# Kernel tuning notes

Hardware: AMD Instinct MI355X
Metric: run time of the kernel (lower is better)

The kernel has to match this reference:

```python
import jax, jax.numpy as jnp
import numpy as np
import math

BIG, SMALL, HEADS, FF_MULT = 4096, 256, 4, 2
HEAD_DIM = SMALL // HEADS
FF = SMALL * FF_MULT
EPS = 1.1920929e-07  # torch.nn.RMSNorm default eps=None -> finfo(float32).eps


def rmsnorm(x, g):
    var = jnp.mean(x * x, axis=-1, keepdims=True)
    return x * jax.lax.rsqrt(var + EPS) * g


def setup_inputs() -> dict:
    key = jax.random.key(0)
    ks = jax.random.split(key, 10)
    B, T = 4, 2048
    def lin(k, out_d, in_d):
        # torch nn.Linear default init: U(-1/sqrt(in), 1/sqrt(in)), weight shape (out, in)
        lim = 1.0 / math.sqrt(in_d)
        return jax.random.uniform(k, (out_d, in_d), jnp.float32, -lim, lim)
    return {
        "x": jax.random.normal(ks[0], (B, T, BIG), jnp.float32),
        "W_down": lin(ks[1], SMALL, BIG),
        "W_up": lin(ks[2], BIG, SMALL),
        "W_qkv": lin(ks[3], 3 * SMALL, SMALL),
        "W_o": lin(ks[4], SMALL, SMALL),
        "W_gate": lin(ks[5], FF, SMALL),
        "W_upff": lin(ks[6], FF, SMALL),
        "W_downff": lin(ks[7], SMALL, FF),
        "g1": jnp.ones((SMALL,), jnp.float32),
        "g2": jnp.ones((SMALL,), jnp.float32),
    }


def reference(x, W_down, W_up, W_qkv, W_o, W_gate, W_upff, W_downff, g1, g2):
    B, T, _ = x.shape
    h = x @ W_down.T                                     # (B,T,small)
    hn = rmsnorm(h, g1)
    qkv = (hn @ W_qkv.T).reshape(B, T, 3, HEADS, HEAD_DIM)
    qkv = jnp.transpose(qkv, (2, 0, 3, 1, 4))            # (3,B,H,T,hd)
    q, k, v = qkv[0], qkv[1], qkv[2]
    scores = jnp.einsum('bhqd,bhkd->bhqk', q, k) / math.sqrt(HEAD_DIM)
    causal = jnp.tril(jnp.ones((T, T), bool))
    scores = jnp.where(causal, scores, -jnp.inf)
    attn = jax.nn.softmax(scores, axis=-1)
    out = jnp.einsum('bhqk,bhkd->bhqd', attn, v)
    out = jnp.transpose(out, (0, 2, 1, 3)).reshape(B, T, SMALL)
    h = h + out @ W_o.T
    hn = rmsnorm(h, g2)
    ff = (jax.nn.silu(hn @ W_gate.T) * (hn @ W_upff.T)) @ W_downff.T
    h = h + ff
    return h @ W_up.T                                    # (B,T,big)
```

## Files before the change

kernel.cpp:

```cpp
#include <hip/hip_runtime.h>
#include <hip/hip_bf16.h>

typedef __bf16 bf16x8 __attribute__((ext_vector_type(8)));
typedef __bf16 bf16x4 __attribute__((ext_vector_type(4)));
typedef float f32x4 __attribute__((ext_vector_type(4)));

#define MFMA_BF16(a, b, c) __builtin_amdgcn_mfma_f32_16x16x32_bf16((a), (b), (c), 0, 0, 0)

__device__ __forceinline__ void g2lds16(void* lds, const void* g) {
  __builtin_amdgcn_global_load_lds(
      (const __attribute__((address_space(1))) void*)g,
      (__attribute__((address_space(3))) void*)lds, 16, 0, 0);
}

enum { EP_BF16 = 0, EP_F32 = 1, EP_ADD_F32 = 2, EP_ADD_BF16OUT = 3 };

template <int EPI, int MT, bool SPLITK = false>
__global__ __launch_bounds__(256, 2) void gemm_nt_kernel(
    const __bf16* __restrict__ A, const __bf16* __restrict__ B, const int K,
    __bf16* __restrict__ Co, float* __restrict__ Cf, const int ldc)
{
  __shared__ __align__(16) __bf16 As[2][MT * 32];
  __shared__ __align__(16) __bf16 Bs[2][128 * 32];
  const int tid = threadIdx.x;
  const int wv = tid >> 6, lane = tid & 63;
  const int r16 = lane & 15, g4 = lane >> 4;
  const int row0 = blockIdx.y * MT, col0 = blockIdx.x * 128;
  const int wr = (MT == 128) ? (wv >> 1) * 64 : 0;
  const int wc = (MT == 128) ? (wv & 1) * 64 : wv * 32;
  constexpr int NW = (MT == 128) ? 4 : 2;
  constexpr int NA = (MT == 128) ? 2 : 1;
  const int kz0 = SPLITK ? blockIdx.z * 512 : 0;

  f32x4 acc[4][NW];
#pragma unroll
  for (int m = 0; m < 4; ++m)
#pragma unroll
    for (int n = 0; n < NW; ++n) acc[m][n] = f32x4{0.f, 0.f, 0.f, 0.f};

  auto stage = [&](int buf, int k0) {
#pragma unroll
    for (int rr = 0; rr < NA; ++rr) {
      const int u = rr * 256 + tid, row = u >> 2, cg = ((u & 3) ^ (row & 3)) * 8;
      g2lds16(&As[buf][u * 8], A + (size_t)(row0 + row) * K + k0 + cg);
    }
#pragma unroll
    for (int rr = 0; rr < 2; ++rr) {
      const int u = rr * 256 + tid, row = u >> 2, cg = ((u & 3) ^ (row & 3)) * 8;
      g2lds16(&Bs[buf][u * 8], B + (size_t)(col0 + row) * K + k0 + cg);
    }
  };

  const int nk = SPLITK ? 16 : (K >> 5);
  const int csw = (g4 ^ (r16 & 3)) * 8;
  int cur = 0;
  stage(0, kz0);
  __syncthreads();

  for (int t = 0; t < nk; ++t) {
    if (t + 1 < nk) stage(cur ^ 1, kz0 + (t + 1) * 32);
    bf16x8 af[4], bfr[NW];
#pragma unroll
    for (int m = 0; m < 4; ++m)
      af[m] = *(const bf16x8*)&As[cur][(wr + m * 16 + r16) * 32 + csw];
#pragma unroll
    for (int n = 0; n < NW; ++n)
      bfr[n] = *(const bf16x8*)&Bs[cur][(wc + n * 16 + r16) * 32 + csw];
#pragma unroll
    for (int m = 0; m < 4; ++m)
#pragma unroll
      for (int n = 0; n < NW; ++n)
        acc[m][n] = MFMA_BF16(af[m], bfr[n], acc[m][n]);
    __syncthreads();
    cur ^= 1;
  }

  const size_t zoff = SPLITK ? (size_t)blockIdx.z * 2097152 : 0;
#pragma unroll
  for (int m = 0; m < 4; ++m)
#pragma unroll
    for (int n = 0; n < NW; ++n)
#pragma unroll
      for (int r = 0; r < 4; ++r) {
        const int row = row0 + wr + m * 16 + g4 * 4 + r;
        const int col = col0 + wc + n * 16 + r16;
        const size_t idx = (size_t)row * ldc + col;
        const float v = acc[m][n][r];
        if constexpr (EPI == EP_BF16) Co[zoff + idx] = (__bf16)v;
        else if constexpr (EPI == EP_F32) Cf[idx] = v;
        else if constexpr (EPI == EP_ADD_F32) Cf[idx] += v;
        else Co[idx] = (__bf16)(Cf[idx] + v);
      }
}

__global__ void cvt_x_kernel(const float* __restrict__ src, __bf16* __restrict__ dst)
{
  const int stride = gridDim.x * 256;
  for (size_t i = (size_t)blockIdx.x * 256 + threadIdx.x; i < 8388608; i += stride) {
    const f32x4 v = *(const f32x4*)(src + i * 4);
    bf16x4 o;
#pragma unroll
    for (int j = 0; j < 4; ++j) o[j] = (__bf16)v[j];
    *(bf16x4*)(dst + i * 4) = o;
  }
}

__global__ void rmsnorm_reduce_kernel(const __bf16* __restrict__ part, const float* __restrict__ g,
                                      float* __restrict__ h, __bf16* __restrict__ out)
{
  const int wv = threadIdx.x >> 6, lane = threadIdx.x & 63;
  const size_t row = (size_t)blockIdx.x * 4 + wv;
  const size_t i = row * 256 + lane * 4;
  f32x4 v = {0.f, 0.f, 0.f, 0.f};
#pragma unroll
  for (int z = 0; z < 8; ++z) {
    const bf16x4 p = *(const bf16x4*)(part + (size_t)z * 2097152 + i);
#pragma unroll
    for (int j = 0; j < 4; ++j) v[j] += (float)p[j];
  }
  *(f32x4*)(h + i) = v;
  float s = v[0] * v[0] + v[1] * v[1] + v[2] * v[2] + v[3] * v[3];
#pragma unroll
  for (int off = 1; off < 64; off <<= 1) s += __shfl_xor(s, off);
  const float scale = rsqrtf(s * (1.f / 256.f) + 1.1920929e-07f);
  const f32x4 gv = *(const f32x4*)(g + lane * 4);
  bf16x4 o;
#pragma unroll
  for (int j = 0; j < 4; ++j) o[j] = (__bf16)(v[j] * scale * gv[j]);
  *(bf16x4*)(out + i) = o;
}

__global__ void rmsnorm_kernel(const float* __restrict__ h, const float* __restrict__ g,
                               __bf16* __restrict__ out)
{
  const int wv = threadIdx.x >> 6, lane = threadIdx.x & 63;
  const size_t row = (size_t)blockIdx.x * 4 + wv;
  const f32x4 v = *(const f32x4*)(h + row * 256 + lane * 4);
  float s = v[0] * v[0] + v[1] * v[1] + v[2] * v[2] + v[3] * v[3];
#pragma unroll
  for (int off = 1; off < 64; off <<= 1) s += __shfl_xor(s, off);
  const float scale = rsqrtf(s * (1.f / 256.f) + 1.1920929e-07f);
  const f32x4 gv = *(const f32x4*)(g + lane * 4);
  bf16x4 o;
#pragma unroll
  for (int j = 0; j < 4; ++j) o[j] = (__bf16)(v[j] * scale * gv[j]);
  *(bf16x4*)(out + row * 256 + lane * 4) = o;
}

struct CvtPack { const float* s[7]; __bf16* d[7]; int n[7]; };
__global__ void cvt_all_kernel(CvtPack p)
{
  int i = (blockIdx.x * 256 + threadIdx.x) * 4;
#pragma unroll
  for (int k = 0; k < 7; ++k) {
    if (i < p.n[k]) {
      const f32x4 v = *(const f32x4*)(p.s[k] + i);
      bf16x4 o;
#pragma unroll
      for (int j = 0; j < 4; ++j) o[j] = (__bf16)v[j];
      *(bf16x4*)(p.d[k] + i) = o;
      return;
    }
    i -= p.n[k];
  }
}

__global__ void silumul_kernel(const __bf16* __restrict__ gu, __bf16* __restrict__ out)
{
  const int gid = blockIdx.x * 256 + threadIdx.x;
  const int row = gid >> 6, k = (gid & 63) * 8;
  const bf16x8 gv = *(const bf16x8*)(gu + (size_t)row * 1024 + k);
  const bf16x8 uv = *(const bf16x8*)(gu + (size_t)row * 1024 + 512 + k);
  bf16x8 ov;
#pragma unroll
  for (int j = 0; j < 8; ++j) {
    const float x = (float)gv[j];
    ov[j] = (__bf16)((x / (1.f + __expf(-x))) * (float)uv[j]);
  }
  *(bf16x8*)(out + (size_t)row * 512 + k) = ov;
}

__global__ __launch_bounds__(256, 4) void attn_kernel(
    const __bf16* __restrict__ qkv, float* __restrict__ opart, float* __restrict__ lpart)
{
  const int bh = blockIdx.x;
  const int by = blockIdx.y;
  const int qb = (by < 16) ? (31 - by) : (by - 16);
  const int z = blockIdx.z;
  const int b = bh >> 2, hh = bh & 3;
  const int tid = threadIdx.x, wv = tid >> 6, lane = tid & 63;
  const int r16 = lane & 15, g4 = lane >> 4;
  const __bf16* base = qkv + (size_t)b * 2048 * 768;
  const int q0 = qb * 64;

  __shared__ __align__(16) __bf16 Ks[2][64 * 64];
  __shared__ __align__(16) __bf16 Vt[64 * 72];
  __shared__ __align__(16) __bf16 Ps[4][16 * 72];

  bf16x8 qf[2];
  {
    const __bf16* qrow = base + (size_t)(q0 + wv * 16 + r16) * 768 + hh * 64;
    qf[0] = *(const bf16x8*)(qrow + g4 * 8);
    qf[1] = *(const bf16x8*)(qrow + 32 + g4 * 8);
  }

  f32x4 oacc[4];
#pragma unroll
  for (int t = 0; t < 4; ++t) oacc[t] = f32x4{0.f, 0.f, 0.f, 0.f};
  float lsum[4] = {0.f, 0.f, 0.f, 0.f};

  auto stageK = [&](int buf, int kv0) {
#pragma unroll
    for (int rr = 0; rr < 2; ++rr) {
      const int u = rr * 256 + tid;
      const int kv = u >> 3, c = u & 7;
      g2lds16(&Ks[buf][u * 8],
              base + (size_t)(kv0 + kv) * 768 + 256 + hh * 64 + ((c ^ (kv & 7)) * 8));
    }
  };
  const int vrow = tid >> 2, vdg = (tid & 3) * 16;
  const int va_ = vrow >> 3, vb_ = vrow & 7;

  bf16x8 v0r, v1r;
  auto loadV = [&](int kv0) {
    const __bf16* vsrc = base + (size_t)(kv0 + vrow) * 768 + 512 + hh * 64 + vdg;
    v0r = *(const bf16x8*)vsrc;
    v1r = *(const bf16x8*)(vsrc + 8);
  };
  auto writeVt = [&]() {
#pragma unroll
    for (int i = 0; i < 8; ++i) {
      int d = vdg + i;
      Vt[d * 72 + ((va_ ^ (d >> 3)) << 3) + vb_] = v0r[i];
      d = vdg + 8 + i;
      Vt[d * 72 + ((va_ ^ (d >> 3)) << 3) + vb_] = v1r[i];
    }
  };

  int c = z, cur = 0;
  const bool any = (c <= qb);
  if (any) { stageK(0, c * 64); loadV(c * 64); }
  __syncthreads();
  if (any) writeVt();
  __syncthreads();

  while (c <= qb) {
    const int nxt = c + 2;
    if (nxt <= qb) { stageK(cur ^ 1, nxt * 64); loadV(nxt * 64); }

    f32x4 sacc[4];
#pragma unroll
    for (int t = 0; t < 4; ++t) sacc[t] = f32x4{0.f, 0.f, 0.f, 0.f};
#pragma unroll
    for (int t = 0; t < 4; ++t)
#pragma unroll
      for (int kk = 0; kk < 2; ++kk) {
        const bf16x8 kf = *(const bf16x8*)
            &Ks[cur][(t * 16 + r16) * 64 + (((kk * 4 + g4) ^ (r16 & 7)) * 8)];
        sacc[t] = MFMA_BF16(qf[kk], kf, sacc[t]);
      }

    const bool diag = (c == qb);
#pragma unroll
    for (int t = 0; t < 4; ++t)
#pragma unroll
      for (int r = 0; r < 4; ++r) {
        float p = __expf(sacc[t][r] * 0.125f);
        if (diag && (t * 16 + r16 > wv * 16 + g4 * 4 + r)) p = 0.f;
        lsum[r] += p;
        Ps[wv][(g4 * 4 + r) * 72 + t * 16 + r16] = (__bf16)p;
      }
    bf16x8 pa[2];
    pa[0] = *(const bf16x8*)&Ps[wv][r16 * 72 + g4 * 8];
    pa[1] = *(const bf16x8*)&Ps[wv][r16 * 72 + 32 + g4 * 8];

#pragma unroll
    for (int t2 = 0; t2 < 4; ++t2)
#pragma unroll
      for (int kk = 0; kk < 2; ++kk) {
        const int d = t2 * 16 + r16;
        const bf16x8 vf = *(const bf16x8*)
            &Vt[d * 72 + (((kk * 4 + g4) ^ (d >> 3)) * 8)];
        oacc[t2] = MFMA_BF16(pa[kk], vf, oacc[t2]);
      }

    __syncthreads();
    if (nxt <= qb) writeVt();
    __syncthreads();
    c = nxt;
    cur ^= 1;
  }

#pragma unroll
  for (int r = 0; r < 4; ++r) {
    lsum[r] += __shfl_xor(lsum[r], 1);
    lsum[r] += __shfl_xor(lsum[r], 2);
    lsum[r] += __shfl_xor(lsum[r], 4);
    lsum[r] += __shfl_xor(lsum[r], 8);
  }
  const size_t pb = (size_t)(bh * 32 + qb) * 2 + z;
  float* op = opart + pb * 4096;
#pragma unroll
  for (int t2 = 0; t2 < 4; ++t2)
#pragma unroll
    for (int r = 0; r < 4; ++r)
      op[(wv * 16 + g4 * 4 + r) * 64 + t2 * 16 + r16] = oacc[t2][r];
  if (r16 == 0) {
    float* lp = lpart + pb * 64;
#pragma unroll
    for (int r = 0; r < 4; ++r) lp[wv * 16 + g4 * 4 + r] = lsum[r];
  }
}

__global__ void attn_merge_kernel(const float* __restrict__ opart,
                                  const float* __restrict__ lpart,
                                  __bf16* __restrict__ ao)
{
  const int gid = blockIdx.x * 256 + threadIdx.x;
  const int col4 = (gid & 63) * 4;
  const int row_t = gid >> 6;
  const int b = row_t >> 11, row = row_t & 2047;
  const int qb = row >> 6, rloc = row & 63;
  const int hh = col4 >> 6, d = col4 & 63;
  const size_t p0 = ((size_t)((b * 4 + hh) * 32 + qb)) * 2;
  const f32x4 o0 = *(const f32x4*)(opart + p0 * 4096 + rloc * 64 + d);
  const f32x4 o1 = *(const f32x4*)(opart + (p0 + 1) * 4096 + rloc * 64 + d);
  const float inv = 1.f / (lpart[p0 * 64 + rloc] + lpart[(p0 + 1) * 64 + rloc]);
  bf16x4 o;
#pragma unroll
  for (int j = 0; j < 4; ++j) o[j] = (__bf16)((o0[j] + o1[j]) * inv);
  *(bf16x4*)(ao + (size_t)row_t * 256 + col4) = o;
}

extern "C" void kernel_launch(void* const* d_in, const int* in_sizes, int n_in,
                              void* d_out, int out_size, void* d_ws, size_t ws_size,
                              hipStream_t stream) {
  (void)in_sizes; (void)n_in; (void)out_size; (void)ws_size;
  const float* x     = (const float*)d_in[0];
  const float* Wdown = (const float*)d_in[1];
  const float* Wup   = (const float*)d_in[2];
  const float* Wqkv  = (const float*)d_in[3];
  const float* Wo    = (const float*)d_in[4];
  const float* Wgate = (const float*)d_in[5];
  const float* Wupff = (const float*)d_in[6];
  const float* Wdff  = (const float*)d_in[7];
  const float* g1    = (const float*)d_in[8];
  const float* g2    = (const float*)d_in[9];
  float* out = (float*)d_out;

  const size_t MB = 1 << 20;
  char* ws = (char*)d_ws;
  float*  h  = (float*)ws;
  __bf16* hn = (__bf16*)(ws + 8 * MB);
  __bf16* ao = (__bf16*)(ws + 12 * MB);
  __bf16* wb_down = (__bf16*)(ws + 16 * MB);
  __bf16* wb_up   = (__bf16*)(ws + 18 * MB);
  __bf16* wb_qkv  = (__bf16*)(ws + 20 * MB);
  __bf16* wb_o    = (__bf16*)(ws + 20 * MB + 384 * 1024);
  __bf16* wb_gate = (__bf16*)(ws + 20 * MB + 512 * 1024);
  __bf16* wb_upff = (__bf16*)(ws + 20 * MB + 768 * 1024);
  __bf16* wb_dff  = (__bf16*)(ws + 21 * MB);
  __bf16* hb = ao;

  char* ob = (char*)d_out;
  __bf16* xb    = (__bf16*)(ob);
  __bf16* hpart = (__bf16*)(ob + 64 * MB);
  __bf16* qkv   = (__bf16*)(ob);
  __bf16* gu    = (__bf16*)(ob + 12 * MB);
  __bf16* ffmid = (__bf16*)(ob + 28 * MB);
  float* opart  = (float*)(ob + 36 * MB);
  float* lpart  = (float*)(ob + 53 * MB);

  CvtPack cp;
  cp.s[0] = Wdown; cp.d[0] = wb_down; cp.n[0] = 1048576;
  cp.s[1] = Wup;   cp.d[1] = wb_up;   cp.n[1] = 1048576;
  cp.s[2] = Wqkv;  cp.d[2] = wb_qkv;  cp.n[2] = 196608;
  cp.s[3] = Wo;    cp.d[3] = wb_o;    cp.n[3] = 65536;
  cp.s[4] = Wgate; cp.d[4] = wb_gate; cp.n[4] = 131072;
  cp.s[5] = Wupff; cp.d[5] = wb_upff; cp.n[5] = 131072;
  cp.s[6] = Wdff;  cp.d[6] = wb_dff;  cp.n[6] = 131072;
  cvt_all_kernel<<<2688, 256, 0, stream>>>(cp);

  cvt_x_kernel<<<2048, 256, 0, stream>>>(x, xb);
  gemm_nt_kernel<EP_BF16, 128, true><<<dim3(2, 64, 8), 256, 0, stream>>>(
      xb, wb_down, 4096, hpart, nullptr, 256);
  rmsnorm_reduce_kernel<<<2048, 256, 0, stream>>>(hpart, g1, h, hn);

  gemm_nt_kernel<EP_BF16, 64><<<dim3(6, 128), 256, 0, stream>>>(
      hn, wb_qkv, 256, qkv, nullptr, 768);
  attn_kernel<<<dim3(16, 32, 2), 256, 0, stream>>>(qkv, opart, lpart);
  attn_merge_kernel<<<2048, 256, 0, stream>>>(opart, lpart, ao);
  gemm_nt_kernel<EP_ADD_F32, 64><<<dim3(2, 128), 256, 0, stream>>>(
      ao, wb_o, 256, nullptr, h, 256);
  rmsnorm_kernel<<<2048, 256, 0, stream>>>(h, g2, hn);
  gemm_nt_kernel<EP_BF16, 64><<<dim3(8, 128), 256, 0, stream>>>(
      hn, wb_gate, 256, gu, nullptr, 1024);
  silumul_kernel<<<2048, 256, 0, stream>>>(gu, ffmid);
  gemm_nt_kernel<EP_ADD_BF16OUT, 64><<<dim3(2, 128), 256, 0, stream>>>(
      ffmid, wb_dff, 512, hb, h, 256);
  gemm_nt_kernel<EP_F32, 128><<<dim3(32, 64), 256, 0, stream>>>(
      hb, wb_up, 256, nullptr, out, 4096);
}
```

Baseline: 213.1 us.

## Fuse attention merge into W_o GEMM, store bf16 partials, halve split-K

Removes the separate attention-merge kernel by merging the two split-KV partial outputs (now stored as bf16) and normalizing them during the A-tile load of a dedicated W_o GEMM. The down-projection split-K factor drops from 8 to 4, so the partial buffer and the reduce traffic shrink while each block runs a longer K loop. The final output GEMM uses nontemporal stores. This trades a kernel launch and fp32 partial traffic for non-async register-staged A loads and a small extra precision loss in the attention partials.

```diff
diff --git a/kernel.cpp b/kernel.cpp
--- a/kernel.cpp
+++ b/kernel.cpp
@@ -30,7 +30,7 @@
   const int wc = (MT == 128) ? (wv & 1) * 64 : wv * 32;
   constexpr int NW = (MT == 128) ? 4 : 2;
   constexpr int NA = (MT == 128) ? 2 : 1;
-  const int kz0 = SPLITK ? blockIdx.z * 512 : 0;
+  const int kz0 = SPLITK ? blockIdx.z * 1024 : 0;
 
   f32x4 acc[4][NW];
 #pragma unroll
@@ -51,7 +51,7 @@
     }
   };
 
-  const int nk = SPLITK ? 16 : (K >> 5);
+  const int nk = SPLITK ? 32 : (K >> 5);
   const int csw = (g4 ^ (r16 & 3)) * 8;
   int cur = 0;
   stage(0, kz0);
@@ -87,9 +87,89 @@
         const size_t idx = (size_t)row * ldc + col;
         const float v = acc[m][n][r];
         if constexpr (EPI == EP_BF16) Co[zoff + idx] = (__bf16)v;
-        else if constexpr (EPI == EP_F32) Cf[idx] = v;
+        else if constexpr (EPI == EP_F32) __builtin_nontemporal_store(v, &Cf[idx]);
         else if constexpr (EPI == EP_ADD_F32) Cf[idx] += v;
         else Co[idx] = (__bf16)(Cf[idx] + v);
+      }
+}
+
+__global__ __launch_bounds__(256, 2) void gemm_wo_kernel(
+    const __bf16* __restrict__ opart, const float* __restrict__ lpart,
+    const __bf16* __restrict__ B, float* __restrict__ Cf)
+{
+  __shared__ __align__(16) __bf16 As[2][64 * 32];
+  __shared__ __align__(16) __bf16 Bs[2][128 * 32];
+  const int tid = threadIdx.x;
+  const int wv = tid >> 6, lane = tid & 63;
+  const int r16 = lane & 15, g4 = lane >> 4;
+  const int row0 = blockIdx.y * 64, col0 = blockIdx.x * 128;
+  const int wc = wv * 32;
+
+  f32x4 acc[4][2];
+#pragma unroll
+  for (int m = 0; m < 4; ++m)
+#pragma unroll
+    for (int n = 0; n < 2; ++n) acc[m][n] = f32x4{0.f, 0.f, 0.f, 0.f};
+
+  const int arow = tid >> 2;
+  const int R = row0 + arow;
+  const int b = R >> 11, rr_ = R & 2047;
+  const int qb = rr_ >> 6, rloc = rr_ & 63;
+  const int cgrp = ((tid & 3) ^ (arow & 3)) * 8;
+
+  auto stageA = [&](int buf, int t) {
+    const int hh = t >> 1;
+    const int dbase = (t & 1) * 32 + cgrp;
+    const size_t pb = ((size_t)((b * 4 + hh) * 32 + qb)) * 2;
+    const bf16x8 o0 = *(const bf16x8*)(opart + pb * 4096 + rloc * 64 + dbase);
+    const bf16x8 o1 = *(const bf16x8*)(opart + (pb + 1) * 4096 + rloc * 64 + dbase);
+    const float inv = 1.f / (lpart[pb * 64 + rloc] + lpart[(pb + 1) * 64 + rloc]);
+    bf16x8 w;
+#pragma unroll
+    for (int j = 0; j < 8; ++j) w[j] = (__bf16)(((float)o0[j] + (float)o1[j]) * inv);
+    *(bf16x8*)&As[buf][tid * 8] = w;
+  };
+  auto stageB = [&](int buf, int k0) {
+#pragma unroll
+    for (int rr = 0; rr < 2; ++rr) {
+      const int u = rr * 256 + tid, row = u >> 2, cg = ((u & 3) ^ (row & 3)) * 8;
+      g2lds16(&Bs[buf][u * 8], B + (size_t)(col0 + row) * 256 + k0 + cg);
+    }
+  };
+
+  const int csw = (g4 ^ (r16 & 3)) * 8;
+  int cur = 0;
+  stageA(0, 0);
+  stageB(0, 0);
+  __syncthreads();
+
+  for (int t = 0; t < 8; ++t) {
+    if (t + 1 < 8) { stageA(cur ^ 1, t + 1); stageB(cur ^ 1, (t + 1) * 32); }
+    bf16x8 af[4], bfr[2];
+#pragma unroll
+    for (int m = 0; m < 4; ++m)
+      af[m] = *(const bf16x8*)&As[cur][(m * 16 + r16) * 32 + csw];
+#pragma unroll
+    for (int n = 0; n < 2; ++n)
+      bfr[n] = *(const bf16x8*)&Bs[cur][(wc + n * 16 + r16) * 32 + csw];
+#pragma unroll
+    for (int m = 0; m < 4; ++m)
+#pragma unroll
+      for (int n = 0; n < 2; ++n)
+        acc[m][n] = MFMA_BF16(af[m], bfr[n], acc[m][n]);
+    __syncthreads();
+    cur ^= 1;
+  }
+
+#pragma unroll
+  for (int m = 0; m < 4; ++m)
+#pragma unroll
+    for (int n = 0; n < 2; ++n)
+#pragma unroll
+      for (int r = 0; r < 4; ++r) {
+        const int row = row0 + m * 16 + g4 * 4 + r;
+        const int col = col0 + wc + n * 16 + r16;
+        Cf[(size_t)row * 256 + col] += acc[m][n][r];
       }
 }
 
@@ -113,7 +193,7 @@
   const size_t i = row * 256 + lane * 4;
   f32x4 v = {0.f, 0.f, 0.f, 0.f};
 #pragma unroll
-  for (int z = 0; z < 8; ++z) {
+  for (int z = 0; z < 4; ++z) {
     const bf16x4 p = *(const bf16x4*)(part + (size_t)z * 2097152 + i);
 #pragma unroll
     for (int j = 0; j < 4; ++j) v[j] += (float)p[j];
@@ -181,7 +261,7 @@
 }
 
 __global__ __launch_bounds__(256, 4) void attn_kernel(
-    const __bf16* __restrict__ qkv, float* __restrict__ opart, float* __restrict__ lpart)
+    const __bf16* __restrict__ qkv, __bf16* __restrict__ opart, float* __restrict__ lpart)
 {
   const int bh = blockIdx.x;
   const int by = blockIdx.y;
@@ -299,37 +379,17 @@
     lsum[r] += __shfl_xor(lsum[r], 8);
   }
   const size_t pb = (size_t)(bh * 32 + qb) * 2 + z;
-  float* op = opart + pb * 4096;
+  __bf16* op = opart + pb * 4096;
 #pragma unroll
   for (int t2 = 0; t2 < 4; ++t2)
 #pragma unroll
     for (int r = 0; r < 4; ++r)
-      op[(wv * 16 + g4 * 4 + r) * 64 + t2 * 16 + r16] = oacc[t2][r];
+      op[(wv * 16 + g4 * 4 + r) * 64 + t2 * 16 + r16] = (__bf16)oacc[t2][r];
   if (r16 == 0) {
     float* lp = lpart + pb * 64;
 #pragma unroll
     for (int r = 0; r < 4; ++r) lp[wv * 16 + g4 * 4 + r] = lsum[r];
   }
-}
-
-__global__ void attn_merge_kernel(const float* __restrict__ opart,
-                                  const float* __restrict__ lpart,
-                                  __bf16* __restrict__ ao)
-{
-  const int gid = blockIdx.x * 256 + threadIdx.x;
-  const int col4 = (gid & 63) * 4;
-  const int row_t = gid >> 6;
-  const int b = row_t >> 11, row = row_t & 2047;
-  const int qb = row >> 6, rloc = row & 63;
-  const int hh = col4 >> 6, d = col4 & 63;
-  const size_t p0 = ((size_t)((b * 4 + hh) * 32 + qb)) * 2;
-  const f32x4 o0 = *(const f32x4*)(opart + p0 * 4096 + rloc * 64 + d);
-  const f32x4 o1 = *(const f32x4*)(opart + (p0 + 1) * 4096 + rloc * 64 + d);
-  const float inv = 1.f / (lpart[p0 * 64 + rloc] + lpart[(p0 + 1) * 64 + rloc]);
-  bf16x4 o;
-#pragma unroll
-  for (int j = 0; j < 4; ++j) o[j] = (__bf16)((o0[j] + o1[j]) * inv);
-  *(bf16x4*)(ao + (size_t)row_t * 256 + col4) = o;
 }
 
 extern "C" void kernel_launch(void* const* d_in, const int* in_sizes, int n_in,
@@ -352,7 +412,7 @@
   char* ws = (char*)d_ws;
   float*  h  = (float*)ws;
   __bf16* hn = (__bf16*)(ws + 8 * MB);
-  __bf16* ao = (__bf16*)(ws + 12 * MB);
+  __bf16* hb = (__bf16*)(ws + 12 * MB);
   __bf16* wb_down = (__bf16*)(ws + 16 * MB);
   __bf16* wb_up   = (__bf16*)(ws + 18 * MB);
   __bf16* wb_qkv  = (__bf16*)(ws + 20 * MB);
@@ -360,7 +420,6 @@
   __bf16* wb_gate = (__bf16*)(ws + 20 * MB + 512 * 1024);
   __bf16* wb_upff = (__bf16*)(ws + 20 * MB + 768 * 1024);
   __bf16* wb_dff  = (__bf16*)(ws + 21 * MB);
-  __bf16* hb = ao;
 
   char* ob = (char*)d_out;
   __bf16* xb    = (__bf16*)(ob);
@@ -368,7 +427,7 @@
   __bf16* qkv   = (__bf16*)(ob);
   __bf16* gu    = (__bf16*)(ob + 12 * MB);
   __bf16* ffmid = (__bf16*)(ob + 28 * MB);
-  float* opart  = (float*)(ob + 36 * MB);
+  __bf16* opart = (__bf16*)(ob + 36 * MB);
   float* lpart  = (float*)(ob + 53 * MB);
 
   CvtPack cp;
@@ -382,16 +441,14 @@
   cvt_all_kernel<<<2688, 256, 0, stream>>>(cp);
 
   cvt_x_kernel<<<2048, 256, 0, stream>>>(x, xb);
-  gemm_nt_kernel<EP_BF16, 128, true><<<dim3(2, 64, 8), 256, 0, stream>>>(
+  gemm_nt_kernel<EP_BF16, 128, true><<<dim3(2, 64, 4), 256, 0, stream>>>(
       xb, wb_down, 4096, hpart, nullptr, 256);
   rmsnorm_reduce_kernel<<<2048, 256, 0, stream>>>(hpart, g1, h, hn);
 
   gemm_nt_kernel<EP_BF16, 64><<<dim3(6, 128), 256, 0, stream>>>(
       hn, wb_qkv, 256, qkv, nullptr, 768);
   attn_kernel<<<dim3(16, 32, 2), 256, 0, stream>>>(qkv, opart, lpart);
-  attn_merge_kernel<<<2048, 256, 0, stream>>>(opart, lpart, ao);
-  gemm_nt_kernel<EP_ADD_F32, 64><<<dim3(2, 128), 256, 0, stream>>>(
-      ao, wb_o, 256, nullptr, h, 256);
+  gemm_wo_kernel<<<dim3(2, 128), 256, 0, stream>>>(opart, lpart, wb_o, h);
   rmsnorm_kernel<<<2048, 256, 0, stream>>>(h, g2, hn);
   gemm_nt_kernel<EP_BF16, 64><<<dim3(8, 128), 256, 0, stream>>>(
       hn, wb_gate, 256, gu, nullptr, 1024);
```

Result: faster. 204.2 us (-4.2%).
